# Optimization experiments

Hardware: AMD Instinct MI355X
Metric: run time of the kernel (lower is better)

## Reference

```python
import jax, jax.numpy as jnp
import numpy as np

N_EMBED = 1024
N_HEADS = 16
HEAD = N_EMBED // N_HEADS
EPS = 1e-5


def setup_inputs() -> dict:
    key = jax.random.key(0)
    ks = jax.random.split(key, 16)
    C = N_EMBED
    s = lambda fan_in: 1.0 / np.sqrt(fan_in)
    return {
        "x": jax.random.normal(ks[0], (4, 2048, C), jnp.float32),
        "ln1_g": jnp.ones((C,), jnp.float32),
        "ln1_b": jnp.zeros((C,), jnp.float32),
        "w_attn": jax.random.normal(ks[1], (C, 3 * C), jnp.float32) * s(C),
        "b_attn": jnp.zeros((3 * C,), jnp.float32),
        "w_proj": jax.random.normal(ks[2], (C, C), jnp.float32) * s(C),
        "b_proj": jnp.zeros((C,), jnp.float32),
        "ln2_g": jnp.ones((C,), jnp.float32),
        "ln2_b": jnp.zeros((C,), jnp.float32),
        "w_fc": jax.random.normal(ks[3], (C, 4 * C), jnp.float32) * s(C),
        "b_fc": jnp.zeros((4 * C,), jnp.float32),
        "w_fc2": jax.random.normal(ks[4], (4 * C, C), jnp.float32) * s(4 * C),
        "b_fc2": jnp.zeros((C,), jnp.float32),
    }


def _layernorm(x, g, b):
    mu = jnp.mean(x, axis=-1, keepdims=True)
    var = jnp.mean(jnp.square(x - mu), axis=-1, keepdims=True)
    return (x - mu) * jax.lax.rsqrt(var + EPS) * g + b


def _attention(x, w_attn, b_attn, w_proj, b_proj):
    B, T, C = x.shape
    qkv = x @ w_attn + b_attn  # [B,T,3C]
    q, k, v = jnp.split(qkv, 3, axis=-1)
    q = q.reshape(B, T, N_HEADS, HEAD).transpose(0, 2, 1, 3)  # [B,H,T,D]
    k = k.reshape(B, T, N_HEADS, HEAD).transpose(0, 2, 1, 3)
    v = v.reshape(B, T, N_HEADS, HEAD).transpose(0, 2, 1, 3)
    scale = 1.0 / np.sqrt(HEAD)
    affin = jnp.einsum("bhqd,bhkd->bhqk", q, k) * scale  # [B,H,T,T]
    causal = jnp.tril(jnp.ones((T, T), bool))
    affin = jnp.where(causal, affin, -jnp.inf)
    affin = jax.nn.softmax(affin, axis=-1)
    y = jnp.einsum("bhqk,bhkd->bhqd", affin, v)  # [B,H,T,D]
    y = y.transpose(0, 2, 1, 3).reshape(B, T, C)
    return y @ w_proj + b_proj


def reference(x, ln1_g, ln1_b, w_attn, b_attn, w_proj, b_proj,
              ln2_g, ln2_b, w_fc, b_fc, w_fc2, b_fc2):
    x = x + _attention(_layernorm(x, ln1_g, ln1_b), w_attn, b_attn, w_proj, b_proj)
    h = _layernorm(x, ln2_g, ln2_b)
    h = jax.nn.gelu(h @ w_fc + b_fc, approximate=True)  # tanh GELU
    x = x + (h @ w_fc2 + b_fc2)
    return x
```

## Files before the change

kernel.cpp:

```cpp
#include <hip/hip_runtime.h>
#include <math.h>


#define M_ROWS 8192
#define T_SEQ 2048
#define N_EMB 1024
#define N_HEADS 16
#define HEAD_D 64

typedef _Float16 f16;
typedef __attribute__((ext_vector_type(8))) _Float16 f16x8;
typedef __attribute__((ext_vector_type(4))) _Float16 f16x4;
typedef __attribute__((ext_vector_type(4))) float f32x4;

__device__ __forceinline__ void async16(void* lds, const void* g) {
    __builtin_amdgcn_global_load_lds(
        (const __attribute__((address_space(1))) unsigned int*)g,
        (__attribute__((address_space(3))) unsigned int*)lds, 16, 0, 0);
}

__device__ __forceinline__ float gelu_tanh(float v) {
    float u = 0.7978845608028654f * (v + 0.044715f * v * v * v);
    float e = __expf(2.0f * u);
    float t = 1.0f - 2.0f / (e + 1.0f);
    return 0.5f * v * (1.0f + t);
}

__launch_bounds__(256)
__global__ void wconv_kernel(const float* __restrict__ W, f16* __restrict__ WT,
                             int K, int N) {
    __shared__ float t[32][33];
    int tx = threadIdx.x & 31, ty = threadIdx.x >> 5;
    int n0 = blockIdx.x * 32, k0 = blockIdx.y * 32;
    #pragma unroll
    for (int r = 0; r < 4; r++)
        t[ty * 4 + r][tx] = W[(size_t)(k0 + ty * 4 + r) * N + n0 + tx];
    __syncthreads();
    #pragma unroll
    for (int r = 0; r < 4; r++)
        WT[(size_t)(n0 + ty * 4 + r) * K + k0 + tx] = (f16)t[tx][ty * 4 + r];
}

__launch_bounds__(256)
__global__ void ln_kernel(const float* __restrict__ x, const float* __restrict__ g,
                          const float* __restrict__ b, f16* __restrict__ y) {
    int row = blockIdx.x;
    int tid = threadIdx.x;
    const float* xr = x + (size_t)row * N_EMB;
    float4 v = *(const float4*)(xr + tid * 4);
    float s  = v.x + v.y + v.z + v.w;
    float sq = v.x * v.x + v.y * v.y + v.z * v.z + v.w * v.w;
    #pragma unroll
    for (int off = 32; off > 0; off >>= 1) {
        s  += __shfl_down(s, off);
        sq += __shfl_down(sq, off);
    }
    __shared__ float ws_[4], wq_[4];
    __shared__ float mean_s, rstd_s;
    int lane = tid & 63, wid = tid >> 6;
    if (lane == 0) { ws_[wid] = s; wq_[wid] = sq; }
    __syncthreads();
    if (tid == 0) {
        float st = ws_[0] + ws_[1] + ws_[2] + ws_[3];
        float qt = wq_[0] + wq_[1] + wq_[2] + wq_[3];
        float mu = st * (1.0f / N_EMB);
        float var = qt * (1.0f / N_EMB) - mu * mu;
        mean_s = mu;
        rstd_s = rsqrtf(var + 1e-5f);
    }
    __syncthreads();
    float mu = mean_s, r = rstd_s;
    float4 gv = *(const float4*)(g + tid * 4);
    float4 bv = *(const float4*)(b + tid * 4);
    f16x4 o;
    o.x = (f16)((v.x - mu) * r * gv.x + bv.x);
    o.y = (f16)((v.y - mu) * r * gv.y + bv.y);
    o.z = (f16)((v.z - mu) * r * gv.z + bv.z);
    o.w = (f16)((v.w - mu) * r * gv.w + bv.w);
    *(f16x4*)(y + (size_t)row * N_EMB + tid * 4) = o;
}

template <int EPI>
__launch_bounds__(256)
__global__ void gemm_f16(const f16* __restrict__ A, const f16* __restrict__ Bt,
                         const float* __restrict__ bias, const float* __restrict__ res,
                         float* __restrict__ Cf, f16* __restrict__ Ch,
                         f16* __restrict__ vT, int K, int N) {
    __shared__ f16 As[2][128 * 32];
    __shared__ f16 Bs[2][128 * 32];
    int tid = threadIdx.x;
    int lane = tid & 63, wave = tid >> 6;
    int wr = wave >> 1, wc = wave & 1;
    int quad = lane >> 4, l16 = lane & 15;
    int m0 = blockIdx.y * 128, n0 = blockIdx.x * 128;

    int r0 = tid >> 2;
    int s0 = (tid & 3) * 8;
    const f16* paA0 = A  + (size_t)(m0 + r0) * K + s0;
    const f16* paA1 = A  + (size_t)(m0 + r0 + 64) * K + s0;
    const f16* paB0 = Bt + (size_t)(n0 + r0) * K + s0;
    const f16* paB1 = Bt + (size_t)(n0 + r0 + 64) * K + s0;
    char* dA0 = (char*)As + (size_t)tid * 16;
    char* dA1 = (char*)As + (size_t)(256 + tid) * 16;
    char* dB0 = (char*)Bs + (size_t)tid * 16;
    char* dB1 = (char*)Bs + (size_t)(256 + tid) * 16;

    async16(dA0, paA0);
    async16(dA1, paA1);
    async16(dB0, paB0);
    async16(dB1, paB1);

    f32x4 acc[4][4] = {};
    int p = 0;
    for (int k0 = 0; k0 < K; k0 += 32, p ^= 1) {
        __syncthreads();
        if (k0 + 32 < K) {
            int koff = k0 + 32;
            async16(dA0 + (p ^ 1) * 8192, paA0 + koff);
            async16(dA1 + (p ^ 1) * 8192, paA1 + koff);
            async16(dB0 + (p ^ 1) * 8192, paB0 + koff);
            async16(dB1 + (p ^ 1) * 8192, paB1 + koff);
        }
        const f16* as = As[p];
        const f16* bs = Bs[p];
        f16x8 af[4], bf[4];
        #pragma unroll
        for (int i = 0; i < 4; i++)
            af[i] = *(const f16x8*)&as[(wr * 64 + i * 16 + l16) * 32 + quad * 8];
        #pragma unroll
        for (int j = 0; j < 4; j++)
            bf[j] = *(const f16x8*)&bs[(wc * 64 + j * 16 + l16) * 32 + quad * 8];
        #pragma unroll
        for (int i = 0; i < 4; i++)
            #pragma unroll
            for (int j = 0; j < 4; j++)
                acc[i][j] = __builtin_amdgcn_mfma_f32_16x16x32_f16(
                    af[i], bf[j], acc[i][j], 0, 0, 0);
    }

    #pragma unroll
    for (int i = 0; i < 4; i++) {
        int row0 = m0 + wr * 64 + i * 16 + quad * 4;
        #pragma unroll
        for (int j = 0; j < 4; j++) {
            int col = n0 + wc * 64 + j * 16 + l16;
            float bb = bias[col];
            if (EPI == 3) {
                if (n0 < 2048) {
                    #pragma unroll
                    for (int r = 0; r < 4; r++)
                        Ch[(size_t)(row0 + r) * 2048 + col] = (f16)(acc[i][j][r] + bb);
                } else {
                    int hh = (col - 2048) >> 6, dd = col & 63;
                    int bb_ = row0 >> 11, t0 = row0 & 2047;
                    f16x4 pk;
                    pk.x = (f16)(acc[i][j][0] + bb);
                    pk.y = (f16)(acc[i][j][1] + bb);
                    pk.z = (f16)(acc[i][j][2] + bb);
                    pk.w = (f16)(acc[i][j][3] + bb);
                    *(f16x4*)(vT + ((size_t)(bb_ * 16 + hh) * 64 + dd) * 2048 + t0) = pk;
                }
            } else {
                #pragma unroll
                for (int r = 0; r < 4; r++) {
                    size_t idx = (size_t)(row0 + r) * N + col;
                    float v = acc[i][j][r] + bb;
                    if (EPI == 1) v += res[idx];
                    if (EPI == 2) Ch[idx] = (f16)gelu_tanh(v);
                    else          Cf[idx] = v;
                }
            }
        }
    }
}

__launch_bounds__(256, 2)
__global__ void flash_kernel(const f16* __restrict__ qk, const f16* __restrict__ vT,
                             f16* __restrict__ y) {
    __shared__ __align__(16) char smem[67584];
    f16* Ks = (f16*)smem;
    f16* Vs = (f16*)(smem + 16384);
    int tid = threadIdx.x;
    int lane = tid & 63, w = tid >> 6;
    int quad = lane >> 4, l16 = lane & 15;
    f16* Ps = (f16*)(smem + 32768 + w * 8704);

    int qt = 15 - blockIdx.x;
    int bh = blockIdx.y;
    int b = bh >> 4, h = bh & 15;
    int q0 = qt * 128;

    f16x8 qf[2][2];
    #pragma unroll
    for (int qn = 0; qn < 2; qn++) {
        int q = q0 + w * 32 + qn * 16 + l16;
        #pragma unroll
        for (int dblk = 0; dblk < 2; dblk++) {
            f16x8 t = *(const f16x8*)(qk + (size_t)(b * T_SEQ + q) * 2048 +
                                      h * 64 + dblk * 32 + quad * 8);
            #pragma unroll
            for (int e = 0; e < 8; e++) t[e] = t[e] * (f16)0.125f;
            qf[qn][dblk] = t;
        }
    }

    float m_r[2] = {-INFINITY, -INFINITY};
    float l_r[2] = {0.0f, 0.0f};
    f32x4 Oacc[2][4] = {};

    for (int jt = 0; jt <= qt; jt++) {
        int j0 = jt * 128;
        __syncthreads();
        #pragma unroll
        for (int i = 0; i < 4; i++) {
            int L = i * 256 + tid;
            int j = L >> 3, g1 = L & 7;
            int g = g1 ^ (j & 7);
            async16((char*)Ks + (size_t)L * 16,
                    qk + (size_t)(b * T_SEQ + j0 + j) * 2048 + 1024 + h * 64 + g * 8);
        }
        #pragma unroll
        for (int i = 0; i < 4; i++) {
            int L = i * 256 + tid;
            int d = L >> 4, g1 = L & 15;
            int g = (g1 & 8) | ((g1 ^ d) & 7);
            async16((char*)Vs + (size_t)L * 16,
                    vT + ((size_t)(bh) * 64 + d) * 2048 + j0 + g * 8);
        }
        __syncthreads();

        f32x4 S[8][2];
        #pragma unroll
        for (int jm = 0; jm < 8; jm++) {
            f16x8 kf[2];
            #pragma unroll
            for (int dblk = 0; dblk < 2; dblk++) {
                int j = jm * 16 + l16;
                int g = (dblk * 4 + quad) ^ (j & 7);
                kf[dblk] = *(const f16x8*)(Ks + (size_t)(j * 8 + g) * 8);
            }
            #pragma unroll
            for (int qn = 0; qn < 2; qn++) {
                f32x4 s = {};
                s = __builtin_amdgcn_mfma_f32_16x16x32_f16(kf[0], qf[qn][0], s, 0, 0, 0);
                s = __builtin_amdgcn_mfma_f32_16x16x32_f16(kf[1], qf[qn][1], s, 0, 0, 0);
                S[jm][qn] = s;
            }
        }

        if (jt == qt) {
            #pragma unroll
            for (int jm = 0; jm < 8; jm++)
                #pragma unroll
                for (int qn = 0; qn < 2; qn++)
                    #pragma unroll
                    for (int r = 0; r < 4; r++) {
                        int jl = jm * 16 + quad * 4 + r;
                        int ql = w * 32 + qn * 16 + l16;
                        if (jl > ql) S[jm][qn][r] = -1e30f;
                    }
        }

        float alpha[2];
        #pragma unroll
        for (int qn = 0; qn < 2; qn++) {
            float tmax = -INFINITY;
            #pragma unroll
            for (int jm = 0; jm < 8; jm++)
                #pragma unroll
                for (int r = 0; r < 4; r++)
                    tmax = fmaxf(tmax, S[jm][qn][r]);
            tmax = fmaxf(tmax, __shfl_xor(tmax, 16));
            tmax = fmaxf(tmax, __shfl_xor(tmax, 32));
            float mnew = fmaxf(m_r[qn], tmax);
            alpha[qn] = __expf(m_r[qn] - mnew);
            m_r[qn] = mnew;
            float rsum = 0.0f;
            #pragma unroll
            for (int jm = 0; jm < 8; jm++)
                #pragma unroll
                for (int r = 0; r < 4; r++) {
                    float p = __expf(S[jm][qn][r] - mnew);
                    S[jm][qn][r] = p;
                    rsum += p;
                }
            rsum += __shfl_xor(rsum, 16);
            rsum += __shfl_xor(rsum, 32);
            l_r[qn] = l_r[qn] * alpha[qn] + rsum;
        }

        #pragma unroll
        for (int jm = 0; jm < 8; jm++)
            #pragma unroll
            for (int qn = 0; qn < 2; qn++) {
                f16x4 pk;
                pk.x = (f16)S[jm][qn][0];
                pk.y = (f16)S[jm][qn][1];
                pk.z = (f16)S[jm][qn][2];
                pk.w = (f16)S[jm][qn][3];
                *(f16x4*)(Ps + (size_t)(qn * 16 + l16) * 136 + jm * 16 + quad * 4) = pk;
            }

        float aPV[2][4];
        #pragma unroll
        for (int m = 0; m < 2; m++)
            #pragma unroll
            for (int r = 0; r < 4; r++)
                aPV[m][r] = __shfl(alpha[m], quad * 20 + r);
        #pragma unroll
        for (int m = 0; m < 2; m++)
            #pragma unroll
            for (int n = 0; n < 4; n++)
                #pragma unroll
                for (int r = 0; r < 4; r++)
                    Oacc[m][n][r] *= aPV[m][r];

        #pragma unroll
        for (int kblk = 0; kblk < 4; kblk++) {
            f16x8 pf[2];
            #pragma unroll
            for (int m = 0; m < 2; m++)
                pf[m] = *(const f16x8*)(Ps + (size_t)(m * 16 + l16) * 136 +
                                        kblk * 32 + quad * 8);
            f16x8 vf[4];
            #pragma unroll
            for (int n = 0; n < 4; n++) {
                int d = n * 16 + l16;
                int g = (kblk * 4 + quad);
                int gs = (g & 8) | ((g ^ d) & 7);
                vf[n] = *(const f16x8*)(Vs + (size_t)(d * 16 + gs) * 8);
            }
            #pragma unroll
            for (int m = 0; m < 2; m++)
                #pragma unroll
                for (int n = 0; n < 4; n++)
                    Oacc[m][n] = __builtin_amdgcn_mfma_f32_16x16x32_f16(
                        pf[m], vf[n], Oacc[m][n], 0, 0, 0);
        }
    }

    #pragma unroll
    for (int m = 0; m < 2; m++) {
        float lPV[4];
        #pragma unroll
        for (int r = 0; r < 4; r++)
            lPV[r] = 1.0f / __shfl(l_r[m], quad * 20 + r);
        #pragma unroll
        for (int n = 0; n < 4; n++) {
            #pragma unroll
            for (int r = 0; r < 4; r++) {
                int q = q0 + w * 32 + m * 16 + quad * 4 + r;
                y[(size_t)(b * T_SEQ + q) * N_EMB + h * 64 + n * 16 + l16] =
                    (f16)(Oacc[m][n][r] * lPV[r]);
            }
        }
    }
}

extern "C" void kernel_launch(void* const* d_in, const int* in_sizes, int n_in,
                              void* d_out, int out_size, void* d_ws, size_t ws_size,
                              hipStream_t stream) {
    const float* x      = (const float*)d_in[0];
    const float* ln1_g  = (const float*)d_in[1];
    const float* ln1_b  = (const float*)d_in[2];
    const float* w_attn = (const float*)d_in[3];
    const float* b_attn = (const float*)d_in[4];
    const float* w_proj = (const float*)d_in[5];
    const float* b_proj = (const float*)d_in[6];
    const float* ln2_g  = (const float*)d_in[7];
    const float* ln2_b  = (const float*)d_in[8];
    const float* w_fc   = (const float*)d_in[9];
    const float* b_fc   = (const float*)d_in[10];
    const float* w_fc2  = (const float*)d_in[11];
    const float* b_fc2  = (const float*)d_in[12];
    float* out = (float*)d_out;

    const size_t MB = 1024 * 1024;
    char* ws = (char*)d_ws;
    f16*   lnbuf = (f16*)ws;
    f16*   qkbuf = (f16*)(ws + 16 * MB);
    f16*   vTbuf = (f16*)(ws + 48 * MB);
    f16*   ybuf  = (f16*)(ws + 64 * MB);
    f16*   h     = (f16*)(ws + 80 * MB);
    f16*   wT    = (f16*)(ws + 144 * MB);
    f16* wT_attn = wT;
    f16* wT_proj = wT_attn + (size_t)3072 * 1024;
    f16* wT_fc   = wT_proj + (size_t)1024 * 1024;
    f16* wT_fc2  = wT_fc   + (size_t)1024 * 4096;

    wconv_kernel<<<dim3(3072 / 32, 1024 / 32), 256, 0, stream>>>(w_attn, wT_attn, 1024, 3072);
    wconv_kernel<<<dim3(1024 / 32, 1024 / 32), 256, 0, stream>>>(w_proj, wT_proj, 1024, 1024);
    wconv_kernel<<<dim3(4096 / 32, 1024 / 32), 256, 0, stream>>>(w_fc,   wT_fc,   1024, 4096);
    wconv_kernel<<<dim3(1024 / 32, 4096 / 32), 256, 0, stream>>>(w_fc2,  wT_fc2,  4096, 1024);

    ln_kernel<<<M_ROWS, 256, 0, stream>>>(x, ln1_g, ln1_b, lnbuf);
    gemm_f16<3><<<dim3(3072 / 128, M_ROWS / 128), 256, 0, stream>>>(
        lnbuf, wT_attn, b_attn, nullptr, nullptr, qkbuf, vTbuf, 1024, 3072);
    flash_kernel<<<dim3(16, 64), 256, 0, stream>>>(qkbuf, vTbuf, ybuf);
    gemm_f16<1><<<dim3(1024 / 128, M_ROWS / 128), 256, 0, stream>>>(
        ybuf, wT_proj, b_proj, x, out, nullptr, nullptr, 1024, 1024);
    ln_kernel<<<M_ROWS, 256, 0, stream>>>(out, ln2_g, ln2_b, lnbuf);
    gemm_f16<2><<<dim3(4096 / 128, M_ROWS / 128), 256, 0, stream>>>(
        lnbuf, wT_fc, b_fc, nullptr, nullptr, h, nullptr, 1024, 4096);
    gemm_f16<1><<<dim3(1024 / 128, M_ROWS / 128), 256, 0, stream>>>(
        h, wT_fc2, b_fc2, out, out, nullptr, nullptr, 4096, 1024);
}
```

Measured before the change: 576.5 us.

## Read K/V tiles directly from global memory in flash attention, drop LDS staging

The flash attention kernel no longer stages K and V tiles in shared memory with async loads and block barriers. Each wave now loads its K and V fragments straight from global memory, relying on L1/L2 reuse, and LDS is kept only for the per-wave P buffer, guarded by waitcnt fences. This removes two __syncthreads per tile and shrinks LDS use, which may raise occupancy, but each of the four waves now loads the same K/V data, so global/cache traffic goes up. The softmax also switches to exp2f by folding log2(e) into the Q scale, and the occupancy hint in launch bounds is dropped.

```diff
diff --git a/kernel.cpp b/kernel.cpp
--- a/kernel.cpp
+++ b/kernel.cpp
@@ -12,6 +12,8 @@
 typedef __attribute__((ext_vector_type(8))) _Float16 f16x8;
 typedef __attribute__((ext_vector_type(4))) _Float16 f16x4;
 typedef __attribute__((ext_vector_type(4))) float f32x4;
+
+#define LDS_FENCE() asm volatile("s_waitcnt lgkmcnt(0)" ::: "memory")
 
 __device__ __forceinline__ void async16(void* lds, const void* g) {
     __builtin_amdgcn_global_load_lds(
@@ -174,32 +176,33 @@
     }
 }
 
-__launch_bounds__(256, 2)
+__launch_bounds__(256)
 __global__ void flash_kernel(const f16* __restrict__ qk, const f16* __restrict__ vT,
                              f16* __restrict__ y) {
-    __shared__ __align__(16) char smem[67584];
-    f16* Ks = (f16*)smem;
-    f16* Vs = (f16*)(smem + 16384);
+    __shared__ __align__(16) f16 PsAll[4][32 * 136];
     int tid = threadIdx.x;
     int lane = tid & 63, w = tid >> 6;
     int quad = lane >> 4, l16 = lane & 15;
-    f16* Ps = (f16*)(smem + 32768 + w * 8704);
+    f16* Ps = PsAll[w];
 
     int qt = 15 - blockIdx.x;
     int bh = blockIdx.y;
     int b = bh >> 4, h = bh & 15;
     int q0 = qt * 128;
-
+    const f16* kbase = qk + (size_t)b * T_SEQ * 2048 + 1024 + h * 64;
+    const f16* vbase = vT + (size_t)bh * 64 * 2048;
+
+    const f16 qsc = (f16)0.1803368801f;
     f16x8 qf[2][2];
     #pragma unroll
     for (int qn = 0; qn < 2; qn++) {
         int q = q0 + w * 32 + qn * 16 + l16;
         #pragma unroll
         for (int dblk = 0; dblk < 2; dblk++) {
-            f16x8 t = *(const f16x8*)(qk + (size_t)(b * T_SEQ + q) * 2048 +
+            f16x8 t = *(const f16x8*)(qk + ((size_t)b * T_SEQ + q) * 2048 +
                                       h * 64 + dblk * 32 + quad * 8);
             #pragma unroll
-            for (int e = 0; e < 8; e++) t[e] = t[e] * (f16)0.125f;
+            for (int e = 0; e < 8; e++) t[e] = t[e] * qsc;
             qf[qn][dblk] = t;
         }
     }
@@ -210,40 +213,18 @@
 
     for (int jt = 0; jt <= qt; jt++) {
         int j0 = jt * 128;
-        __syncthreads();
-        #pragma unroll
-        for (int i = 0; i < 4; i++) {
-            int L = i * 256 + tid;
-            int j = L >> 3, g1 = L & 7;
-            int g = g1 ^ (j & 7);
-            async16((char*)Ks + (size_t)L * 16,
-                    qk + (size_t)(b * T_SEQ + j0 + j) * 2048 + 1024 + h * 64 + g * 8);
-        }
-        #pragma unroll
-        for (int i = 0; i < 4; i++) {
-            int L = i * 256 + tid;
-            int d = L >> 4, g1 = L & 15;
-            int g = (g1 & 8) | ((g1 ^ d) & 7);
-            async16((char*)Vs + (size_t)L * 16,
-                    vT + ((size_t)(bh) * 64 + d) * 2048 + j0 + g * 8);
-        }
-        __syncthreads();
 
         f32x4 S[8][2];
         #pragma unroll
         for (int jm = 0; jm < 8; jm++) {
-            f16x8 kf[2];
-            #pragma unroll
-            for (int dblk = 0; dblk < 2; dblk++) {
-                int j = jm * 16 + l16;
-                int g = (dblk * 4 + quad) ^ (j & 7);
-                kf[dblk] = *(const f16x8*)(Ks + (size_t)(j * 8 + g) * 8);
-            }
+            const f16* krow = kbase + (size_t)(j0 + jm * 16 + l16) * 2048 + quad * 8;
+            f16x8 kf0 = *(const f16x8*)krow;
+            f16x8 kf1 = *(const f16x8*)(krow + 32);
             #pragma unroll
             for (int qn = 0; qn < 2; qn++) {
                 f32x4 s = {};
-                s = __builtin_amdgcn_mfma_f32_16x16x32_f16(kf[0], qf[qn][0], s, 0, 0, 0);
-                s = __builtin_amdgcn_mfma_f32_16x16x32_f16(kf[1], qf[qn][1], s, 0, 0, 0);
+                s = __builtin_amdgcn_mfma_f32_16x16x32_f16(kf0, qf[qn][0], s, 0, 0, 0);
+                s = __builtin_amdgcn_mfma_f32_16x16x32_f16(kf1, qf[qn][1], s, 0, 0, 0);
                 S[jm][qn] = s;
             }
         }
@@ -273,21 +254,23 @@
             tmax = fmaxf(tmax, __shfl_xor(tmax, 16));
             tmax = fmaxf(tmax, __shfl_xor(tmax, 32));
             float mnew = fmaxf(m_r[qn], tmax);
-            alpha[qn] = __expf(m_r[qn] - mnew);
+            alpha[qn] = exp2f(m_r[qn] - mnew);
             m_r[qn] = mnew;
             float rsum = 0.0f;
             #pragma unroll
             for (int jm = 0; jm < 8; jm++)
                 #pragma unroll
                 for (int r = 0; r < 4; r++) {
-                    float p = __expf(S[jm][qn][r] - mnew);
-                    S[jm][qn][r] = p;
-                    rsum += p;
+                    float pp = exp2f(S[jm][qn][r] - mnew);
+                    S[jm][qn][r] = pp;
+                    rsum += pp;
                 }
             rsum += __shfl_xor(rsum, 16);
             rsum += __shfl_xor(rsum, 32);
             l_r[qn] = l_r[qn] * alpha[qn] + rsum;
         }
+
+        LDS_FENCE();
 
         #pragma unroll
         for (int jm = 0; jm < 8; jm++)
@@ -301,6 +284,8 @@
                 *(f16x4*)(Ps + (size_t)(qn * 16 + l16) * 136 + jm * 16 + quad * 4) = pk;
             }
 
+        LDS_FENCE();
+
         float aPV[2][4];
         #pragma unroll
         for (int m = 0; m < 2; m++)
@@ -324,12 +309,9 @@
                                         kblk * 32 + quad * 8);
             f16x8 vf[4];
             #pragma unroll
-            for (int n = 0; n < 4; n++) {
-                int d = n * 16 + l16;
-                int g = (kblk * 4 + quad);
-                int gs = (g & 8) | ((g ^ d) & 7);
-                vf[n] = *(const f16x8*)(Vs + (size_t)(d * 16 + gs) * 8);
-            }
+            for (int n = 0; n < 4; n++)
+                vf[n] = *(const f16x8*)(vbase + (size_t)(n * 16 + l16) * 2048 +
+                                        j0 + kblk * 32 + quad * 8);
             #pragma unroll
             for (int m = 0; m < 2; m++)
                 #pragma unroll
```

After: 774.3 us. +34.3%, slower.

## Halve per-wave P staging buffer in flash attention and switch softmax to exp2

Applied to the files above, without the earlier changes.

The flash kernel now stages the probability tile P in two halves of 64 keys each. Each half is written to LDS and consumed by the PV MFMAs before the next half is written, with explicit lgkmcnt waits between the steps. This cuts per-wave P storage by half and total shared memory from about 66KB to 50KB, so more blocks can be resident per CU; the launch-bounds minimum of 2 blocks is also dropped. log2(e) is folded into the Q pre-scale so softmax can use exp2f instead of __expf, and the alpha rescale of O is moved before the P writes. The cost is extra LDS waits and serialization between the two halves.

```diff
diff --git a/kernel.cpp b/kernel.cpp
--- a/kernel.cpp
+++ b/kernel.cpp
@@ -12,6 +12,8 @@
 typedef __attribute__((ext_vector_type(8))) _Float16 f16x8;
 typedef __attribute__((ext_vector_type(4))) _Float16 f16x4;
 typedef __attribute__((ext_vector_type(4))) float f32x4;
+
+#define LDS_FENCE() asm volatile("s_waitcnt lgkmcnt(0)" ::: "memory")
 
 __device__ __forceinline__ void async16(void* lds, const void* g) {
     __builtin_amdgcn_global_load_lds(
@@ -174,32 +176,34 @@
     }
 }
 
-__launch_bounds__(256, 2)
+__launch_bounds__(256)
 __global__ void flash_kernel(const f16* __restrict__ qk, const f16* __restrict__ vT,
                              f16* __restrict__ y) {
-    __shared__ __align__(16) char smem[67584];
+    __shared__ __align__(16) char smem[51200];
     f16* Ks = (f16*)smem;
     f16* Vs = (f16*)(smem + 16384);
     int tid = threadIdx.x;
     int lane = tid & 63, w = tid >> 6;
     int quad = lane >> 4, l16 = lane & 15;
-    f16* Ps = (f16*)(smem + 32768 + w * 8704);
+    f16* Ps = (f16*)(smem + 32768 + w * 4608);
 
     int qt = 15 - blockIdx.x;
     int bh = blockIdx.y;
     int b = bh >> 4, h = bh & 15;
     int q0 = qt * 128;
-
+    const size_t qkrow = (size_t)b * T_SEQ * 2048;
+
+    const f16 qsc = (f16)0.1803368801f;
     f16x8 qf[2][2];
     #pragma unroll
     for (int qn = 0; qn < 2; qn++) {
         int q = q0 + w * 32 + qn * 16 + l16;
         #pragma unroll
         for (int dblk = 0; dblk < 2; dblk++) {
-            f16x8 t = *(const f16x8*)(qk + (size_t)(b * T_SEQ + q) * 2048 +
+            f16x8 t = *(const f16x8*)(qk + qkrow + (size_t)q * 2048 +
                                       h * 64 + dblk * 32 + quad * 8);
             #pragma unroll
-            for (int e = 0; e < 8; e++) t[e] = t[e] * (f16)0.125f;
+            for (int e = 0; e < 8; e++) t[e] = t[e] * qsc;
             qf[qn][dblk] = t;
         }
     }
@@ -217,7 +221,7 @@
             int j = L >> 3, g1 = L & 7;
             int g = g1 ^ (j & 7);
             async16((char*)Ks + (size_t)L * 16,
-                    qk + (size_t)(b * T_SEQ + j0 + j) * 2048 + 1024 + h * 64 + g * 8);
+                    qk + qkrow + (size_t)(j0 + j) * 2048 + 1024 + h * 64 + g * 8);
         }
         #pragma unroll
         for (int i = 0; i < 4; i++) {
@@ -225,7 +229,7 @@
             int d = L >> 4, g1 = L & 15;
             int g = (g1 & 8) | ((g1 ^ d) & 7);
             async16((char*)Vs + (size_t)L * 16,
-                    vT + ((size_t)(bh) * 64 + d) * 2048 + j0 + g * 8);
+                    vT + ((size_t)bh * 64 + d) * 2048 + j0 + g * 8);
         }
         __syncthreads();
 
@@ -273,24 +277,38 @@
             tmax = fmaxf(tmax, __shfl_xor(tmax, 16));
             tmax = fmaxf(tmax, __shfl_xor(tmax, 32));
             float mnew = fmaxf(m_r[qn], tmax);
-            alpha[qn] = __expf(m_r[qn] - mnew);
+            alpha[qn] = exp2f(m_r[qn] - mnew);
             m_r[qn] = mnew;
             float rsum = 0.0f;
             #pragma unroll
             for (int jm = 0; jm < 8; jm++)
                 #pragma unroll
                 for (int r = 0; r < 4; r++) {
-                    float p = __expf(S[jm][qn][r] - mnew);
-                    S[jm][qn][r] = p;
-                    rsum += p;
+                    float pp = exp2f(S[jm][qn][r] - mnew);
+                    S[jm][qn][r] = pp;
+                    rsum += pp;
                 }
             rsum += __shfl_xor(rsum, 16);
             rsum += __shfl_xor(rsum, 32);
             l_r[qn] = l_r[qn] * alpha[qn] + rsum;
         }
 
-        #pragma unroll
-        for (int jm = 0; jm < 8; jm++)
+        float aPV[2][4];
+        #pragma unroll
+        for (int m = 0; m < 2; m++)
+            #pragma unroll
+            for (int r = 0; r < 4; r++)
+                aPV[m][r] = __shfl(alpha[m], quad * 20 + r);
+        #pragma unroll
+        for (int m = 0; m < 2; m++)
+            #pragma unroll
+            for (int n = 0; n < 4; n++)
+                #pragma unroll
+                for (int r = 0; r < 4; r++)
+                    Oacc[m][n][r] *= aPV[m][r];
+
+        #pragma unroll
+        for (int jm = 0; jm < 4; jm++)
             #pragma unroll
             for (int qn = 0; qn < 2; qn++) {
                 f16x4 pk;
@@ -298,35 +316,57 @@
                 pk.y = (f16)S[jm][qn][1];
                 pk.z = (f16)S[jm][qn][2];
                 pk.w = (f16)S[jm][qn][3];
-                *(f16x4*)(Ps + (size_t)(qn * 16 + l16) * 136 + jm * 16 + quad * 4) = pk;
-            }
-
-        float aPV[2][4];
-        #pragma unroll
-        for (int m = 0; m < 2; m++)
-            #pragma unroll
-            for (int r = 0; r < 4; r++)
-                aPV[m][r] = __shfl(alpha[m], quad * 20 + r);
-        #pragma unroll
-        for (int m = 0; m < 2; m++)
-            #pragma unroll
-            for (int n = 0; n < 4; n++)
-                #pragma unroll
-                for (int r = 0; r < 4; r++)
-                    Oacc[m][n][r] *= aPV[m][r];
-
-        #pragma unroll
-        for (int kblk = 0; kblk < 4; kblk++) {
+                *(f16x4*)(Ps + (size_t)(qn * 16 + l16) * 72 + jm * 16 + quad * 4) = pk;
+            }
+        LDS_FENCE();
+        #pragma unroll
+        for (int kblk = 0; kblk < 2; kblk++) {
             f16x8 pf[2];
             #pragma unroll
             for (int m = 0; m < 2; m++)
-                pf[m] = *(const f16x8*)(Ps + (size_t)(m * 16 + l16) * 136 +
+                pf[m] = *(const f16x8*)(Ps + (size_t)(m * 16 + l16) * 72 +
                                         kblk * 32 + quad * 8);
             f16x8 vf[4];
             #pragma unroll
             for (int n = 0; n < 4; n++) {
                 int d = n * 16 + l16;
-                int g = (kblk * 4 + quad);
+                int g = kblk * 4 + quad;
+                int gs = (g & 8) | ((g ^ d) & 7);
+                vf[n] = *(const f16x8*)(Vs + (size_t)(d * 16 + gs) * 8);
+            }
+            #pragma unroll
+            for (int m = 0; m < 2; m++)
+                #pragma unroll
+                for (int n = 0; n < 4; n++)
+                    Oacc[m][n] = __builtin_amdgcn_mfma_f32_16x16x32_f16(
+                        pf[m], vf[n], Oacc[m][n], 0, 0, 0);
+        }
+        LDS_FENCE();
+
+        #pragma unroll
+        for (int jm = 4; jm < 8; jm++)
+            #pragma unroll
+            for (int qn = 0; qn < 2; qn++) {
+                f16x4 pk;
+                pk.x = (f16)S[jm][qn][0];
+                pk.y = (f16)S[jm][qn][1];
+                pk.z = (f16)S[jm][qn][2];
+                pk.w = (f16)S[jm][qn][3];
+                *(f16x4*)(Ps + (size_t)(qn * 16 + l16) * 72 + (jm - 4) * 16 + quad * 4) = pk;
+            }
+        LDS_FENCE();
+        #pragma unroll
+        for (int kblk = 2; kblk < 4; kblk++) {
+            f16x8 pf[2];
+            #pragma unroll
+            for (int m = 0; m < 2; m++)
+                pf[m] = *(const f16x8*)(Ps + (size_t)(m * 16 + l16) * 72 +
+                                        (kblk - 2) * 32 + quad * 8);
+            f16x8 vf[4];
+            #pragma unroll
+            for (int n = 0; n < 4; n++) {
+                int d = n * 16 + l16;
+                int g = kblk * 4 + quad;
                 int gs = (g & 8) | ((g ^ d) & 7);
                 vf[n] = *(const f16x8*)(Vs + (size_t)(d * 16 + gs) * 8);
             }
```

After: 678.3 us. 17.6% more time.
